# Performance work log

Hardware: AMD Instinct MI355X
Metric: run time of the kernel (lower is better)

The kernel has to match this reference:

```python
import jax, jax.numpy as jnp
import numpy as np

D_MODEL = 1024
D_STATE = 16
D_CONV = 4
EXPAND = 2
D_INNER = EXPAND * D_MODEL          # 2048
DT_RANK = D_INNER // 16             # 128
BATCH = 2
SEQLEN = 1024


def _silu(x):
    return x * jax.nn.sigmoid(x)


def setup_inputs() -> dict:
    key = jax.random.key(0)
    ks = jax.random.split(key, 8)
    s = 0.02
    A_init = jnp.tile(jnp.arange(1, D_STATE + 1, dtype=jnp.float32)[None, :], (D_INNER, 1))
    return {
        "x": jax.random.normal(ks[0], (BATCH, SEQLEN, D_MODEL), jnp.float32),
        "W_in": jax.random.normal(ks[1], (D_MODEL, 2 * D_INNER), jnp.float32) * s,
        "conv_k": jax.random.normal(ks[2], (D_CONV, 1, D_INNER), jnp.float32) * s,  # (kw, in/groups, out)
        "conv_b": jnp.zeros((D_INNER,), jnp.float32),
        "W_xproj": jax.random.normal(ks[3], (D_INNER, DT_RANK + 2 * D_STATE), jnp.float32) * s,
        "W_dt": jax.random.normal(ks[4], (DT_RANK, D_INNER), jnp.float32) * s,
        "b_dt": jnp.zeros((D_INNER,), jnp.float32),
        "A_log": jnp.log(A_init),
        "D": jnp.ones((D_INNER,), jnp.float32),
        "W_out": jax.random.normal(ks[5], (D_INNER, D_MODEL), jnp.float32) * s,
    }


def reference(x, W_in, conv_k, conv_b, W_xproj, W_dt, b_dt, A_log, D, W_out):
    # in_proj and gate split
    xz = x @ W_in                                   # (B, L, 2*Di)
    x_in, z = jnp.split(xz, 2, axis=-1)             # each (B, L, Di)

    # depthwise causal conv1d: left-pad by d_conv-1 (keras padding='causal')
    xp = jnp.pad(x_in, ((0, 0), (D_CONV - 1, 0), (0, 0)))
    x_in = jax.lax.conv_general_dilated(
        xp, conv_k, window_strides=(1,), padding='VALID',
        dimension_numbers=('NWC', 'WIO', 'NWC'),
        feature_group_count=D_INNER) + conv_b
    u = _silu(x_in)                                 # (B, L, Di)

    # input-dependent SSM params
    x_dbl = u @ W_xproj                             # (B, L, dt_rank + 2*N)
    dt_low, Bm, Cm = jnp.split(x_dbl, [DT_RANK, DT_RANK + D_STATE], axis=-1)
    dt = jax.nn.softplus(dt_low @ W_dt + b_dt)      # (B, L, Di)
    A = -jnp.exp(A_log)                             # (Di, N)
    dA = jnp.exp(jnp.einsum('bld,dn->bldn', dt, A)) # (B, L, Di, N)
    dB = jnp.einsum('bld,bln->bldn', dt, Bm)        # (B, L, Di, N)

    # selective scan over sequence length
    def step(h, e):
        a_t, b_t, u_t, c_t = e                      # (B,Di,N), (B,Di,N), (B,Di), (B,N)
        h = a_t * h + b_t * u_t[..., None]
        y_t = jnp.einsum('bdn,bn->bd', h, c_t)
        return h, y_t

    h0 = jnp.zeros((x.shape[0], D_INNER, D_STATE), dtype=x.dtype)
    xs = (jnp.swapaxes(dA, 0, 1), jnp.swapaxes(dB, 0, 1),
          jnp.swapaxes(u, 0, 1), jnp.swapaxes(Cm, 0, 1))
    _, yT = jax.lax.scan(step, h0, xs)              # (L, B, Di)
    y = jnp.swapaxes(yT, 0, 1) + u * D              # skip connection

    return (y * _silu(z)) @ W_out                   # (B, L, d_model)
```

## Files before the change

### kernel.cpp

```cpp
#include <hip/hip_runtime.h>
#include <hip/hip_bf16.h>

#define D_MODEL 1024
#define D_STATE 16
#define D_CONV 4
#define D_INNER 2048
#define DT_RANK 128
#define BATCH 2
#define SEQLEN 1024
#define XCOLS 160
#define NCHUNK 64
#define LCHUNK 16

typedef __hip_bfloat16 bf16;
typedef __attribute__((ext_vector_type(8))) short short8;
typedef __attribute__((ext_vector_type(4))) float f32x4;

__device__ __forceinline__ unsigned short f2bf_bits(float f) {
    bf16 h = __float2bfloat16(f);
    return *(unsigned short*)&h;
}

__device__ __forceinline__ float softplus_f(float x) {
    return fmaxf(x, 0.f) + __logf(1.f + __expf(-fabsf(x)));
}

__device__ __forceinline__ void load16_lds(void* lds, const void* g) {
    __builtin_amdgcn_global_load_lds(
        (const __attribute__((address_space(1))) unsigned int*)g,
        (__attribute__((address_space(3))) unsigned int*)lds, 16, 0, 0);
}

__device__ __forceinline__ void transpose_tile(const float* __restrict__ B,
                                               bf16* __restrict__ Bt,
                                               int K, int N, int nt, int kt,
                                               float (*t)[33], int tid)
{
    const int tx = tid & 31, ty = tid >> 5;
    const int n0 = nt * 32, k0 = kt * 32;
    #pragma unroll
    for (int r = 0; r < 4; ++r) {
        int n = n0 + tx;
        t[ty + r * 8][tx] = (n < N) ? B[(size_t)(k0 + ty + r * 8) * N + n] : 0.f;
    }
    __syncthreads();
    #pragma unroll
    for (int r = 0; r < 4; ++r)
        Bt[(size_t)(n0 + ty + r * 8) * K + k0 + tx] = __float2bfloat16(t[tx][ty + r * 8]);
}

__global__ __launch_bounds__(256)
void prep_kernel(const float* __restrict__ x, bf16* __restrict__ x_bf,
                 const float* __restrict__ W_in, bf16* __restrict__ Win_t,
                 const float* __restrict__ W_xproj, bf16* __restrict__ Wxp_t,
                 const float* __restrict__ W_dt, bf16* __restrict__ Wdt_t,
                 const float* __restrict__ W_out, bf16* __restrict__ Wout_t,
                 const float* __restrict__ A_log, float* __restrict__ Aneg)
{
    __shared__ float t[32][33];
    const int tid = threadIdx.x;
    int blk = blockIdx.x;
    if (blk < 4096) {
        transpose_tile(W_in, Win_t, D_MODEL, 2 * D_INNER, blk & 127, blk >> 7, t, tid);
        return;
    }
    blk -= 4096;
    if (blk < 512) {
        transpose_tile(W_xproj, Wxp_t, D_INNER, XCOLS, blk & 7, blk >> 3, t, tid);
        return;
    }
    blk -= 512;
    if (blk < 256) {
        transpose_tile(W_dt, Wdt_t, DT_RANK, D_INNER, blk & 63, blk >> 6, t, tid);
        return;
    }
    blk -= 256;
    if (blk < 2048) {
        transpose_tile(W_out, Wout_t, D_INNER, D_MODEL, blk & 31, blk >> 5, t, tid);
        return;
    }
    blk -= 2048;
    if (blk < 2048) {
        int i = blk * 256 + tid;
        float4 v = ((const float4*)x)[i];
        ushort4 p;
        p.x = f2bf_bits(v.x); p.y = f2bf_bits(v.y);
        p.z = f2bf_bits(v.z); p.w = f2bf_bits(v.w);
        ((ushort4*)x_bf)[i] = p;
        return;
    }
    blk -= 2048;
    {
        int i = blk * 256 + tid;
        Aneg[i] = -__expf(A_log[i]);
    }
}

template<int BN, int EPI>
__global__ __launch_bounds__(256)
void gemm_mfma(const bf16* __restrict__ A, const bf16* __restrict__ Bt,
               float* __restrict__ C, bf16* __restrict__ Cb,
               const float* __restrict__ bias,
               int M, int N, int K, int ldc, int kchunk)
{
    constexpr int WN = (BN == 128) ? 64 : 32;
    constexpr int NJ = WN / 16;
    __shared__ short As[128 * 32];
    __shared__ short Bs[BN * 32];
    const int tid = threadIdx.x;
    const int lane = tid & 63, wave = tid >> 6;
    const int wm = (wave >> 1) * 64, wn = (wave & 1) * WN;
    const int row0 = blockIdx.y * 128, col0 = blockIdx.x * BN;
    const int r_m = lane & 15, r_q = lane >> 4;
    const int kstart = blockIdx.z * kchunk;
    float* Cz = C + (size_t)blockIdx.z * M * ldc;

    const int srow = tid >> 2, schk = (tid & 3) * 8;
    const bf16* Ag0 = A  + (size_t)(row0 + srow)      * K + kstart + schk;
    const bf16* Ag1 = A  + (size_t)(row0 + srow + 64) * K + kstart + schk;
    const bf16* Bg0 = Bt + (size_t)(col0 + srow)      * K + kstart + schk;
    const bf16* Bg1 = Bt + (size_t)(col0 + srow + 64) * K + kstart + schk;
    short* AsW0 = &As[8 * tid];
    short* AsW1 = &As[8 * tid + 2048];
    short* BsW0 = &Bs[8 * tid];
    short* BsW1 = &Bs[8 * tid + 2048];

    f32x4 acc[4][NJ];
    #pragma unroll
    for (int i = 0; i < 4; ++i)
        #pragma unroll
        for (int j = 0; j < NJ; ++j)
            #pragma unroll
            for (int r = 0; r < 4; ++r) acc[i][j][r] = 0.f;

    for (int k0 = 0; k0 < kchunk; k0 += 32) {
        __syncthreads();
        load16_lds(AsW0, Ag0 + k0);
        load16_lds(AsW1, Ag1 + k0);
        load16_lds(BsW0, Bg0 + k0);
        if (BN == 128) load16_lds(BsW1, Bg1 + k0);
        __syncthreads();
        short8 af[4], bfr[NJ];
        #pragma unroll
        for (int i = 0; i < 4; ++i)
            af[i] = *(const short8*)&As[(wm + i * 16 + r_m) * 32 + r_q * 8];
        #pragma unroll
        for (int j = 0; j < NJ; ++j)
            bfr[j] = *(const short8*)&Bs[(wn + j * 16 + r_m) * 32 + r_q * 8];
        #pragma unroll
        for (int i = 0; i < 4; ++i)
            #pragma unroll
            for (int j = 0; j < NJ; ++j)
                acc[i][j] = __builtin_amdgcn_mfma_f32_16x16x32_bf16(
                    af[i], bfr[j], acc[i][j], 0, 0, 0);
    }

    #pragma unroll
    for (int i = 0; i < 4; ++i) {
        #pragma unroll
        for (int j = 0; j < NJ; ++j) {
            int row = row0 + wm + i * 16 + r_q * 4;
            int col = col0 + wn + j * 16 + r_m;
            if (col < N) {
                if (EPI == 1) {
                    float bv = bias[col];
                    #pragma unroll
                    for (int r = 0; r < 4; ++r)
                        Cb[(size_t)(row + r) * ldc + col] =
                            __float2bfloat16(softplus_f(acc[i][j][r] + bv));
                } else {
                    #pragma unroll
                    for (int r = 0; r < 4; ++r)
                        Cz[(size_t)(row + r) * ldc + col] = acc[i][j][r];
                }
            }
        }
    }
}

__global__ __launch_bounds__(256)
void reduce_xdbl(const float* __restrict__ Cpart, float* __restrict__ x_dbl,
                 bf16* __restrict__ dtA_bf)
{
    int i = blockIdx.x * 256 + threadIdx.x;
    if (i >= 2048 * XCOLS) return;
    int r = i / XCOLS, c = i - r * XCOLS;
    float s = 0.f;
    #pragma unroll
    for (int z = 0; z < 8; ++z)
        s += Cpart[(size_t)z * 2048 * 256 + (size_t)r * 256 + c];
    x_dbl[i] = s;
    if (c < DT_RANK) dtA_bf[(size_t)r * DT_RANK + c] = __float2bfloat16(s);
}

__global__ __launch_bounds__(256)
void reduce_out(const float* __restrict__ Cpart, float* __restrict__ out)
{
    int i = blockIdx.x * 256 + threadIdx.x;
    const float4* p0 = (const float4*)Cpart;
    const float4* p1 = p0 + (size_t)2048 * 1024 / 4;
    float4 a = p0[i], b = p1[i];
    float4 r; r.x = a.x + b.x; r.y = a.y + b.y; r.z = a.z + b.z; r.w = a.w + b.w;
    ((float4*)out)[i] = r;
}

__global__ __launch_bounds__(256)
void conv_silu_kernel(const float* __restrict__ xz,
                      const float* __restrict__ conv_k,
                      const float* __restrict__ conv_b,
                      bf16* __restrict__ u_bf)
{
    int idx4 = blockIdx.x * 256 + threadIdx.x;
    int d4 = idx4 & (D_INNER / 4 - 1);
    int t = (idx4 >> 9) & (SEQLEN - 1);
    int b = idx4 >> 19;
    float4 acc = ((const float4*)conv_b)[d4];
    #pragma unroll
    for (int k = 0; k < D_CONV; ++k) {
        int tt = t + k - (D_CONV - 1);
        if (tt >= 0) {
            float4 xv = ((const float4*)xz)[(size_t)(b * SEQLEN + tt) * (2 * D_INNER / 4) + d4];
            float4 kv = ((const float4*)conv_k)[k * (D_INNER / 4) + d4];
            acc.x = fmaf(xv.x, kv.x, acc.x);
            acc.y = fmaf(xv.y, kv.y, acc.y);
            acc.z = fmaf(xv.z, kv.z, acc.z);
            acc.w = fmaf(xv.w, kv.w, acc.w);
        }
    }
    ushort4 pk;
    pk.x = f2bf_bits(acc.x / (1.f + __expf(-acc.x)));
    pk.y = f2bf_bits(acc.y / (1.f + __expf(-acc.y)));
    pk.z = f2bf_bits(acc.z / (1.f + __expf(-acc.z)));
    pk.w = f2bf_bits(acc.w / (1.f + __expf(-acc.w)));
    ((ushort4*)u_bf)[idx4] = pk;
}

__global__ __launch_bounds__(256)
void scan_phase1(const bf16* __restrict__ dt_sb,
                 const float* __restrict__ Aneg,
                 const bf16* __restrict__ u_bf,
                 const float* __restrict__ x_dbl,
                 float* __restrict__ Pst, float* __restrict__ Sst)
{
    __shared__ float Bsm[LCHUNK][16];
    const int d = blockIdx.x * 256 + threadIdx.x;
    const int c = blockIdx.y, b = blockIdx.z;
    const int t0 = c * LCHUNK;
    {
        int tt = threadIdx.x >> 4, n = threadIdx.x & 15;
        Bsm[tt][n] = x_dbl[(size_t)(b * SEQLEN + t0 + tt) * XCOLS + DT_RANK + n];
    }
    float A_row[D_STATE];
    const float4* a4 = (const float4*)(Aneg + d * D_STATE);
    #pragma unroll
    for (int q = 0; q < 4; ++q) {
        float4 v = a4[q];
        A_row[q*4+0] = v.x; A_row[q*4+1] = v.y; A_row[q*4+2] = v.z; A_row[q*4+3] = v.w;
    }
    __syncthreads();
    float P[D_STATE], S[D_STATE];
    #pragma unroll
    for (int n = 0; n < D_STATE; ++n) { P[n] = 1.f; S[n] = 0.f; }
    const bf16* dpp = dt_sb + (size_t)(b * SEQLEN + t0) * D_INNER + d;
    const bf16* upp = u_bf + (size_t)(b * SEQLEN + t0) * D_INNER + d;
    #pragma unroll
    for (int t = 0; t < LCHUNK; ++t) {
        float dtv = __bfloat162float(dpp[(size_t)t * D_INNER]);
        float du = dtv * __bfloat162float(upp[(size_t)t * D_INNER]);
        const float4* b4 = (const float4*)&Bsm[t][0];
        #pragma unroll
        for (int q = 0; q < 4; ++q) {
            float4 v = b4[q];
            float Bn[4] = {v.x, v.y, v.z, v.w};
            #pragma unroll
            for (int e = 0; e < 4; ++e) {
                int n = q * 4 + e;
                float a = __expf(dtv * A_row[n]);
                P[n] *= a;
                S[n] = fmaf(a, S[n], du * Bn[e]);
            }
        }
    }
    const size_t base = ((size_t)(b * NCHUNK + c) * D_STATE) * D_INNER + d;
    #pragma unroll
    for (int n = 0; n < D_STATE; ++n) {
        Pst[base + (size_t)n * D_INNER] = P[n];
        Sst[base + (size_t)n * D_INNER] = S[n];
    }
}

__global__ __launch_bounds__(256)
void scan_phase2(const float* __restrict__ Pst, float* __restrict__ Sst)
{
    const int d = blockIdx.x * 256 + threadIdx.x;
    const int n = blockIdx.y;
    const int b = blockIdx.z;
    float h = 0.f;
    for (int c = 0; c < NCHUNK; ++c) {
        const size_t idx = ((size_t)(b * NCHUNK + c) * D_STATE + n) * D_INNER + d;
        float Pv = Pst[idx], Sv = Sst[idx];
        Sst[idx] = h;
        h = fmaf(Pv, h, Sv);
    }
}

__global__ __launch_bounds__(256)
void scan_phase3(const bf16* __restrict__ dt_sb,
                 const float* __restrict__ Aneg,
                 const bf16* __restrict__ u_bf,
                 const float* __restrict__ x_dbl,
                 const float* __restrict__ Dvec,
                 const float* __restrict__ xz,
                 const float* __restrict__ hin,
                 bf16* __restrict__ g_bf)
{
    __shared__ float BCs[LCHUNK][32];
    const int d = blockIdx.x * 256 + threadIdx.x;
    const int c = blockIdx.y, b = blockIdx.z;
    const int t0 = c * LCHUNK;
    {
        int i0 = threadIdx.x;
        int tt = i0 >> 5, col = i0 & 31;
        BCs[tt][col] = x_dbl[(size_t)(b * SEQLEN + t0 + tt) * XCOLS + DT_RANK + col];
        int i1 = i0 + 256;
        tt = i1 >> 5; col = i1 & 31;
        BCs[tt][col] = x_dbl[(size_t)(b * SEQLEN + t0 + tt) * XCOLS + DT_RANK + col];
    }
    float A_row[D_STATE];
    const float4* a4 = (const float4*)(Aneg + d * D_STATE);
    #pragma unroll
    for (int q = 0; q < 4; ++q) {
        float4 v = a4[q];
        A_row[q*4+0] = v.x; A_row[q*4+1] = v.y; A_row[q*4+2] = v.z; A_row[q*4+3] = v.w;
    }
    const float Dd = Dvec[d];
    __syncthreads();
    float h[D_STATE];
    const size_t base = ((size_t)(b * NCHUNK + c) * D_STATE) * D_INNER + d;
    #pragma unroll
    for (int n = 0; n < D_STATE; ++n) h[n] = hin[base + (size_t)n * D_INNER];
    const bf16* dpp = dt_sb + (size_t)(b * SEQLEN + t0) * D_INNER + d;
    const bf16* upp = u_bf + (size_t)(b * SEQLEN + t0) * D_INNER + d;
    const float* zpp = xz + (size_t)(b * SEQLEN + t0) * (2 * D_INNER) + D_INNER + d;
    bf16* gpp = g_bf + (size_t)(b * SEQLEN + t0) * D_INNER + d;
    #pragma unroll
    for (int t = 0; t < LCHUNK; ++t) {
        float dtv = __bfloat162float(dpp[(size_t)t * D_INNER]);
        float uv = __bfloat162float(upp[(size_t)t * D_INNER]);
        float zv = zpp[(size_t)t * 2 * D_INNER];
        float du = dtv * uv;
        float y = 0.f;
        const float4* bc4 = (const float4*)&BCs[t][0];
        #pragma unroll
        for (int q = 0; q < 4; ++q) {
            float4 v = bc4[q];
            float4 w = bc4[q + 4];
            float Bn[4] = {v.x, v.y, v.z, v.w};
            float Cn[4] = {w.x, w.y, w.z, w.w};
            #pragma unroll
            for (int e = 0; e < 4; ++e) {
                int n = q * 4 + e;
                float a = __expf(dtv * A_row[n]);
                h[n] = fmaf(a, h[n], du * Bn[e]);
                y = fmaf(h[n], Cn[e], y);
            }
        }
        float gy = y + uv * Dd;
        float sz = zv / (1.f + __expf(-zv));
        gpp[(size_t)t * D_INNER] = __float2bfloat16(gy * sz);
    }
}

extern "C" void kernel_launch(void* const* d_in, const int* in_sizes, int n_in,
                              void* d_out, int out_size, void* d_ws, size_t ws_size,
                              hipStream_t stream)
{
    const float* x      = (const float*)d_in[0];
    const float* W_in   = (const float*)d_in[1];
    const float* conv_k = (const float*)d_in[2];
    const float* conv_b = (const float*)d_in[3];
    const float* W_xproj= (const float*)d_in[4];
    const float* W_dt   = (const float*)d_in[5];
    const float* b_dt   = (const float*)d_in[6];
    const float* A_log  = (const float*)d_in[7];
    const float* Dvec   = (const float*)d_in[8];
    const float* W_out  = (const float*)d_in[9];
    float* out = (float*)d_out;

    const int BL = BATCH * SEQLEN;

    float* ws     = (float*)d_ws;
    float* xz     = ws;
    float* x_dbl  = xz     + (size_t)BL * 2 * D_INNER;
    float* Pst    = x_dbl  + (size_t)BL * XCOLS;
    float* Sst    = Pst    + (size_t)BATCH * NCHUNK * D_STATE * D_INNER;
    float* Aneg   = Sst    + (size_t)BATCH * NCHUNK * D_STATE * D_INNER;
    float* Cpart3 = Pst;
    float* Cpart6 = Pst;
    bf16*  x_bf   = (bf16*)Sst;
    bf16* Win_t  = (bf16*)(Aneg + 32768);
    bf16* u_bf   = Win_t + (size_t)4096 * 1024;
    bf16* Wxp_t  = u_bf  + (size_t)BL * D_INNER;
    bf16* dtA_bf = Wxp_t + (size_t)256 * 2048;
    bf16* Wdt_t  = dtA_bf+ (size_t)BL * DT_RANK;
    bf16* g_bf   = Wdt_t + (size_t)2048 * 128;
    bf16* Wout_t = g_bf  + (size_t)BL * D_INNER;
    bf16* dt_sb  = Wout_t+ (size_t)1024 * 2048;

    prep_kernel<<<4096 + 512 + 256 + 2048 + 2048 + 128, 256, 0, stream>>>(
        x, x_bf, W_in, Win_t, W_xproj, Wxp_t, W_dt, Wdt_t, W_out, Wout_t, A_log, Aneg);

    gemm_mfma<128, 0><<<dim3(32, 16, 1), 256, 0, stream>>>(
        x_bf, Win_t, xz, nullptr, nullptr, BL, 2 * D_INNER, D_MODEL, 2 * D_INNER, D_MODEL);

    conv_silu_kernel<<<(BL * D_INNER / 4) / 256, 256, 0, stream>>>(xz, conv_k, conv_b, u_bf);

    gemm_mfma<64, 0><<<dim3(4, 16, 8), 256, 0, stream>>>(
        u_bf, Wxp_t, Cpart3, nullptr, nullptr, BL, 256, D_INNER, 256, 256);
    reduce_xdbl<<<(BL * XCOLS + 255) / 256, 256, 0, stream>>>(Cpart3, x_dbl, dtA_bf);

    gemm_mfma<64, 1><<<dim3(32, 16, 1), 256, 0, stream>>>(
        dtA_bf, Wdt_t, nullptr, dt_sb, b_dt, BL, D_INNER, DT_RANK, D_INNER, DT_RANK);

    scan_phase1<<<dim3(D_INNER / 256, NCHUNK, BATCH), 256, 0, stream>>>(
        dt_sb, Aneg, u_bf, x_dbl, Pst, Sst);
    scan_phase2<<<dim3(D_INNER / 256, D_STATE, BATCH), 256, 0, stream>>>(Pst, Sst);
    scan_phase3<<<dim3(D_INNER / 256, NCHUNK, BATCH), 256, 0, stream>>>(
        dt_sb, Aneg, u_bf, x_dbl, Dvec, xz, Sst, g_bf);

    gemm_mfma<64, 0><<<dim3(16, 16, 2), 256, 0, stream>>>(
        g_bf, Wout_t, Cpart6, nullptr, nullptr, BL, D_MODEL, D_INNER, D_MODEL, D_MODEL);
    reduce_out<<<(BL * D_MODEL / 4) / 256, 256, 0, stream>>>(Cpart6, out);
}
```

Before: 235.8 us.

## Store gate z as bf16 from in_proj epilogue and use larger scan chunks

The in_proj GEMM gets a new epilogue that writes the x half in fp32 to a compact buffer and the z half directly as bf16. The conv and scan_phase3 kernels then read the narrower buffers, which cuts scan_phase3's z read traffic in half. Scan chunking changes from 64 chunks of 16 to 32 chunks of 32. This halves the blocks in phases 1 and 3 and the serial length of phase 2, but gives less parallelism per phase and longer per-thread loops. The workspace layout is reshuffled so x_bf no longer aliases Sst.

```diff
diff --git a/kernel.cpp b/kernel.cpp
--- a/kernel.cpp
+++ b/kernel.cpp
@@ -9,8 +9,8 @@
 #define BATCH 2
 #define SEQLEN 1024
 #define XCOLS 160
-#define NCHUNK 64
-#define LCHUNK 16
+#define NCHUNK 32
+#define LCHUNK 32
 
 typedef __hip_bfloat16 bf16;
 typedef __attribute__((ext_vector_type(8))) short short8;
@@ -168,6 +168,17 @@
                     for (int r = 0; r < 4; ++r)
                         Cb[(size_t)(row + r) * ldc + col] =
                             __float2bfloat16(softplus_f(acc[i][j][r] + bv));
+                } else if (EPI == 2) {
+                    if (col < D_INNER) {
+                        #pragma unroll
+                        for (int r = 0; r < 4; ++r)
+                            Cz[(size_t)(row + r) * D_INNER + col] = acc[i][j][r];
+                    } else {
+                        #pragma unroll
+                        for (int r = 0; r < 4; ++r)
+                            Cb[(size_t)(row + r) * D_INNER + (col - D_INNER)] =
+                                __float2bfloat16(acc[i][j][r]);
+                    }
                 } else {
                     #pragma unroll
                     for (int r = 0; r < 4; ++r)
@@ -205,7 +216,7 @@
 }
 
 __global__ __launch_bounds__(256)
-void conv_silu_kernel(const float* __restrict__ xz,
+void conv_silu_kernel(const float* __restrict__ xz32,
                       const float* __restrict__ conv_k,
                       const float* __restrict__ conv_b,
                       bf16* __restrict__ u_bf)
@@ -219,7 +230,7 @@
     for (int k = 0; k < D_CONV; ++k) {
         int tt = t + k - (D_CONV - 1);
         if (tt >= 0) {
-            float4 xv = ((const float4*)xz)[(size_t)(b * SEQLEN + tt) * (2 * D_INNER / 4) + d4];
+            float4 xv = ((const float4*)xz32)[(size_t)(b * SEQLEN + tt) * (D_INNER / 4) + d4];
             float4 kv = ((const float4*)conv_k)[k * (D_INNER / 4) + d4];
             acc.x = fmaf(xv.x, kv.x, acc.x);
             acc.y = fmaf(xv.y, kv.y, acc.y);
@@ -246,8 +257,8 @@
     const int d = blockIdx.x * 256 + threadIdx.x;
     const int c = blockIdx.y, b = blockIdx.z;
     const int t0 = c * LCHUNK;
-    {
-        int tt = threadIdx.x >> 4, n = threadIdx.x & 15;
+    for (int i = threadIdx.x; i < LCHUNK * 16; i += 256) {
+        int tt = i >> 4, n = i & 15;
         Bsm[tt][n] = x_dbl[(size_t)(b * SEQLEN + t0 + tt) * XCOLS + DT_RANK + n];
     }
     float A_row[D_STATE];
@@ -263,7 +274,7 @@
     for (int n = 0; n < D_STATE; ++n) { P[n] = 1.f; S[n] = 0.f; }
     const bf16* dpp = dt_sb + (size_t)(b * SEQLEN + t0) * D_INNER + d;
     const bf16* upp = u_bf + (size_t)(b * SEQLEN + t0) * D_INNER + d;
-    #pragma unroll
+    #pragma unroll 8
     for (int t = 0; t < LCHUNK; ++t) {
         float dtv = __bfloat162float(dpp[(size_t)t * D_INNER]);
         float du = dtv * __bfloat162float(upp[(size_t)t * D_INNER]);
@@ -310,7 +321,7 @@
                  const bf16* __restrict__ u_bf,
                  const float* __restrict__ x_dbl,
                  const float* __restrict__ Dvec,
-                 const float* __restrict__ xz,
+                 const bf16* __restrict__ z_bf,
                  const float* __restrict__ hin,
                  bf16* __restrict__ g_bf)
 {
@@ -318,12 +329,8 @@
     const int d = blockIdx.x * 256 + threadIdx.x;
     const int c = blockIdx.y, b = blockIdx.z;
     const int t0 = c * LCHUNK;
-    {
-        int i0 = threadIdx.x;
-        int tt = i0 >> 5, col = i0 & 31;
-        BCs[tt][col] = x_dbl[(size_t)(b * SEQLEN + t0 + tt) * XCOLS + DT_RANK + col];
-        int i1 = i0 + 256;
-        tt = i1 >> 5; col = i1 & 31;
+    for (int i = threadIdx.x; i < LCHUNK * 32; i += 256) {
+        int tt = i >> 5, col = i & 31;
         BCs[tt][col] = x_dbl[(size_t)(b * SEQLEN + t0 + tt) * XCOLS + DT_RANK + col];
     }
     float A_row[D_STATE];
@@ -341,13 +348,13 @@
     for (int n = 0; n < D_STATE; ++n) h[n] = hin[base + (size_t)n * D_INNER];
     const bf16* dpp = dt_sb + (size_t)(b * SEQLEN + t0) * D_INNER + d;
     const bf16* upp = u_bf + (size_t)(b * SEQLEN + t0) * D_INNER + d;
-    const float* zpp = xz + (size_t)(b * SEQLEN + t0) * (2 * D_INNER) + D_INNER + d;
+    const bf16* zpp = z_bf + (size_t)(b * SEQLEN + t0) * D_INNER + d;
     bf16* gpp = g_bf + (size_t)(b * SEQLEN + t0) * D_INNER + d;
-    #pragma unroll
+    #pragma unroll 8
     for (int t = 0; t < LCHUNK; ++t) {
         float dtv = __bfloat162float(dpp[(size_t)t * D_INNER]);
         float uv = __bfloat162float(upp[(size_t)t * D_INNER]);
-        float zv = zpp[(size_t)t * 2 * D_INNER];
+        float zv = __bfloat162float(zpp[(size_t)t * D_INNER]);
         float du = dtv * uv;
         float y = 0.f;
         const float4* bc4 = (const float4*)&BCs[t][0];
@@ -388,16 +395,18 @@
     float* out = (float*)d_out;
 
     const int BL = BATCH * SEQLEN;
+    const size_t PS_ELEMS = (size_t)BATCH * NCHUNK * D_STATE * D_INNER;
 
     float* ws     = (float*)d_ws;
-    float* xz     = ws;
-    float* x_dbl  = xz     + (size_t)BL * 2 * D_INNER;
+    float* xz32   = ws;
+    float* x_dbl  = xz32   + (size_t)BL * D_INNER;
     float* Pst    = x_dbl  + (size_t)BL * XCOLS;
-    float* Sst    = Pst    + (size_t)BATCH * NCHUNK * D_STATE * D_INNER;
-    float* Aneg   = Sst    + (size_t)BATCH * NCHUNK * D_STATE * D_INNER;
+    float* Sst    = Pst    + PS_ELEMS;
+    float* extraC = Sst    + PS_ELEMS;
+    float* Aneg   = extraC + (size_t)4194304;
     float* Cpart3 = Pst;
     float* Cpart6 = Pst;
-    bf16*  x_bf   = (bf16*)Sst;
+    bf16*  x_bf   = (bf16*)extraC;
     bf16* Win_t  = (bf16*)(Aneg + 32768);
     bf16* u_bf   = Win_t + (size_t)4096 * 1024;
     bf16* Wxp_t  = u_bf  + (size_t)BL * D_INNER;
@@ -406,14 +415,15 @@
     bf16* g_bf   = Wdt_t + (size_t)2048 * 128;
     bf16* Wout_t = g_bf  + (size_t)BL * D_INNER;
     bf16* dt_sb  = Wout_t+ (size_t)1024 * 2048;
+    bf16* z_bf   = dt_sb + (size_t)BL * D_INNER;
 
     prep_kernel<<<4096 + 512 + 256 + 2048 + 2048 + 128, 256, 0, stream>>>(
         x, x_bf, W_in, Win_t, W_xproj, Wxp_t, W_dt, Wdt_t, W_out, Wout_t, A_log, Aneg);
 
-    gemm_mfma<128, 0><<<dim3(32, 16, 1), 256, 0, stream>>>(
-        x_bf, Win_t, xz, nullptr, nullptr, BL, 2 * D_INNER, D_MODEL, 2 * D_INNER, D_MODEL);
-
-    conv_silu_kernel<<<(BL * D_INNER / 4) / 256, 256, 0, stream>>>(xz, conv_k, conv_b, u_bf);
+    gemm_mfma<128, 2><<<dim3(32, 16, 1), 256, 0, stream>>>(
+        x_bf, Win_t, xz32, z_bf, nullptr, BL, 2 * D_INNER, D_MODEL, D_INNER, D_MODEL);
+
+    conv_silu_kernel<<<(BL * D_INNER / 4) / 256, 256, 0, stream>>>(xz32, conv_k, conv_b, u_bf);
 
     gemm_mfma<64, 0><<<dim3(4, 16, 8), 256, 0, stream>>>(
         u_bf, Wxp_t, Cpart3, nullptr, nullptr, BL, 256, D_INNER, 256, 256);
@@ -426,7 +436,7 @@
         dt_sb, Aneg, u_bf, x_dbl, Pst, Sst);
     scan_phase2<<<dim3(D_INNER / 256, D_STATE, BATCH), 256, 0, stream>>>(Pst, Sst);
     scan_phase3<<<dim3(D_INNER / 256, NCHUNK, BATCH), 256, 0, stream>>>(
-        dt_sb, Aneg, u_bf, x_dbl, Dvec, xz, Sst, g_bf);
+        dt_sb, Aneg, u_bf, x_dbl, Dvec, z_bf, Sst, g_bf);
 
     gemm_mfma<64, 0><<<dim3(16, 16, 2), 256, 0, stream>>>(
         g_bf, Wout_t, Cpart6, nullptr, nullptr, BL, D_MODEL, D_INNER, D_MODEL, D_MODEL);
```

New measurement: 255.9 us. +8.5%, slower.
